# Kernel optimization log

Hardware: AMD Instinct MI355X
Metric: run time of the kernel (lower is better)

The kernel has to match this reference:

```python
import jax, jax.numpy as jnp
import numpy as np

B, S, D, H = 4, 2048, 1024, 16
HD = D // H

def setup_inputs() -> dict:
    key = jax.random.key(0)
    ks = jax.random.split(key, 11)
    s = 1.0 / np.sqrt(D)
    return {
        "q": jax.random.normal(ks[0], (B, S, D), jnp.float32),
        "k": jax.random.normal(ks[1], (B, S, D), jnp.float32),
        "v": jax.random.normal(ks[2], (B, S, D), jnp.float32),
        "Wq": jax.random.normal(ks[3], (D, D), jnp.float32) * s,
        "bq": jax.random.normal(ks[4], (D,), jnp.float32) * 0.01,
        "Wk": jax.random.normal(ks[5], (D, D), jnp.float32) * s,
        "bk": jax.random.normal(ks[6], (D,), jnp.float32) * 0.01,
        "Wv": jax.random.normal(ks[7], (D, D), jnp.float32) * s,
        "bv": jax.random.normal(ks[8], (D,), jnp.float32) * 0.01,
        "Wo": jax.random.normal(ks[9], (D, D), jnp.float32) * s,
        "bo": jax.random.normal(ks[10], (D,), jnp.float32) * 0.01,
    }

def reference(q, k, v, Wq, bq, Wk, bk, Wv, bv, Wo, bo):
    # linear projections + ReLU activation (as in the torch module)
    qh = jax.nn.relu(q @ Wq.T + bq)
    kh = jax.nn.relu(k @ Wk.T + bk)
    vh = jax.nn.relu(v @ Wv.T + bv)
    # split heads: [B,S,D] -> [B,H,S,HD]
    def split(x):
        return x.reshape(B, S, H, HD).transpose(0, 2, 1, 3)
    qh, kh, vh = split(qh), split(kh), split(vh)
    scale = 1.0 / np.sqrt(HD).astype(np.float32)
    scores = jnp.einsum("bhqd,bhkd->bhqk", qh, kh) * scale
    attn = jax.nn.softmax(scores, axis=-1)
    y = jnp.einsum("bhqk,bhkd->bhqd", attn, vh)
    # merge heads: [B,H,S,HD] -> [B,S,D]
    y = y.transpose(0, 2, 1, 3).reshape(B, S, D)
    return jax.nn.relu(y @ Wo.T + bo)
```

## Files before the change

kernel.cpp:

```cpp
#include <hip/hip_runtime.h>
#include <hip/hip_bf16.h>
#include <cstdint>
#include <cstddef>

#define Bc 4
#define Sc 2048
#define Dc 1024
#define Hc 16

typedef __bf16 bf16;
typedef bf16  bf16x4 __attribute__((ext_vector_type(4)));
typedef bf16  bf16x8 __attribute__((ext_vector_type(8)));
typedef float f32x4  __attribute__((ext_vector_type(4)));

__device__ __forceinline__ void load_lds16(const bf16* g, bf16* l) {
    __builtin_amdgcn_global_load_lds((const __attribute__((address_space(1))) void*)g,
                                     (__attribute__((address_space(3))) void*)l,
                                     16, 0, 0);
}

__device__ __forceinline__ void cvt16(const float* __restrict__ g,
                                      bf16x8& lo, bf16x8& hi) {
    const f32x4 a0 = *(const f32x4*)(g);
    const f32x4 a1 = *(const f32x4*)(g + 4);
    const f32x4 a2 = *(const f32x4*)(g + 8);
    const f32x4 a3 = *(const f32x4*)(g + 12);
#pragma unroll
    for (int j = 0; j < 4; j++) {
        lo[j]     = (bf16)a0[j];
        lo[j + 4] = (bf16)a1[j];
        hi[j]     = (bf16)a2[j];
        hi[j + 4] = (bf16)a3[j];
    }
}

__device__ __forceinline__ void store_relu(float* p, float v) { *p = fmaxf(v, 0.0f); }
__device__ __forceinline__ void store_relu(bf16*  p, float v) { *p = (bf16)fmaxf(v, 0.0f); }

__global__ __launch_bounds__(256)
void cvt_f32_bf16(const float* __restrict__ src, bf16* __restrict__ dst, int n16) {
    const int idx = blockIdx.x * 256 + threadIdx.x;
    if (idx >= n16) return;
    bf16x8 lo, hi;
    cvt16(src + (size_t)idx * 16, lo, hi);
    *(bf16x8*)(dst + (size_t)idx * 16)     = lo;
    *(bf16x8*)(dst + (size_t)idx * 16 + 8) = hi;
}

#define BM 128
#define BN 128
#define BK 64

template <typename TC, bool TR>
__global__ __launch_bounds__(256)
void gemm_bb(const bf16* __restrict__ A, const bf16* __restrict__ W,
             const float* __restrict__ bias, TC* __restrict__ C,
             int M, int N, int K) {
    constexpr int POOL = TR ? 36864 : 32768;
    __shared__ __align__(16) char pool[POOL];
    bf16* lA = (bf16*)pool;
    bf16* lB = (bf16*)(pool + 16384);

    const int t    = threadIdx.x;
    const int lane = t & 63;
    const int wave = t >> 6;
    const int l15  = lane & 15;
    const int quad = lane >> 4;

    const int m0 = blockIdx.x * BM;
    const int n0 = blockIdx.y * BN;
    const int wm = (wave >> 1) * 64;
    const int wn = (wave & 1) * 64;

    f32x4 acc[4][4] = {};

    const int srow = t >> 3;
    const int cg   = (((t & 7) ^ (srow & 7)) << 3);
    const bf16* gA = A + (size_t)(m0 + srow) * K + cg;
    const bf16* gW = W + (size_t)(n0 + srow) * K + cg;
    bf16* lA0 = lA + t * 8;
    bf16* lB0 = lB + t * 8;

    for (int k0 = 0; k0 < K; k0 += BK) {
        __syncthreads();
#pragma unroll
        for (int c = 0; c < 4; c++) {
            load_lds16(gA + (size_t)(32 * c) * K, lA0 + c * 2048);
            load_lds16(gW + (size_t)(32 * c) * K, lB0 + c * 2048);
        }
        gA += BK; gW += BK;
        __syncthreads();

#pragma unroll
        for (int ks = 0; ks < 2; ks++) {
            bf16x8 af[4], bfr[4];
#pragma unroll
            for (int mt = 0; mt < 4; mt++) {
                const int row = wm + mt * 16 + l15;
                const int colp = ((((ks << 2) | quad) ^ (l15 & 7)) << 3);
                af[mt] = *(const bf16x8*)(lA + row * BK + colp);
            }
#pragma unroll
            for (int nt = 0; nt < 4; nt++) {
                const int row = wn + nt * 16 + l15;
                const int colp = ((((ks << 2) | quad) ^ (l15 & 7)) << 3);
                bfr[nt] = *(const bf16x8*)(lB + row * BK + colp);
            }
#pragma unroll
            for (int mt = 0; mt < 4; mt++)
#pragma unroll
                for (int nt = 0; nt < 4; nt++)
                    acc[mt][nt] = __builtin_amdgcn_mfma_f32_16x16x32_bf16(
                        af[mt], bfr[nt], acc[mt][nt], 0, 0, 0);
        }
    }

    if constexpr (!TR) {
#pragma unroll
        for (int nt = 0; nt < 4; nt++) {
            const int col = n0 + wn + nt * 16 + l15;
            const float bv = bias[col];
#pragma unroll
            for (int mt = 0; mt < 4; mt++) {
                const int rowb = m0 + wm + mt * 16 + quad * 4;
#pragma unroll
                for (int i = 0; i < 4; i++)
                    store_relu(&C[(size_t)(rowb + i) * N + col], acc[mt][nt][i] + bv);
            }
        }
    } else {
        __syncthreads();
        bf16* trp = (bf16*)pool;
#pragma unroll
        for (int nt = 0; nt < 4; nt++) {
            const int col = n0 + wn + nt * 16 + l15;
            const float bv = bias[col];
#pragma unroll
            for (int mt = 0; mt < 4; mt++)
#pragma unroll
                for (int i = 0; i < 4; i++)
                    trp[((wave * 64) + nt * 16 + l15) * 72 + mt * 16 + quad * 4 + i] =
                        (bf16)fmaxf(acc[mt][nt][i] + bv, 0.0f);
        }
        __syncthreads();
        const int r2 = lane >> 3;
        const int c8 = (lane & 7) * 8;
#pragma unroll
        for (int rr = 0; rr < 8; rr++) {
            const int rt = rr * 8 + r2;
            const bf16x8 vv = *(const bf16x8*)&trp[((wave * 64) + rt) * 72 + c8];
            const int cg2 = n0 + wn + rt;
            const int h   = cg2 >> 6, hd = cg2 & 63;
            const int mg  = m0 + wm + c8;
            const int b   = mg >> 11, s = mg & (Sc - 1);
            bf16* dst = (bf16*)C + ((size_t)(b * Hc + h) * 64 + hd) * Sc + s;
            *(bf16x8*)dst = vv;
        }
    }
}

#define QI 4

__global__ __launch_bounds__(256)
void attn_flash(const bf16* __restrict__ Qh, const bf16* __restrict__ Kh,
                const bf16* __restrict__ Vt_g, bf16* __restrict__ Y) {
    __shared__ __align__(16) bf16 Kl[64][72];
    __shared__ __align__(16) bf16 Vl[64][72];
    __shared__ __align__(16) bf16 Pl[4][64][72];

    const int t    = threadIdx.x;
    const int lane = t & 63;
    const int wave = t >> 6;
    const int l15  = lane & 15;
    const int quad = lane >> 4;

    const int qt = blockIdx.x;
    const int bh = blockIdx.y;
    const int b  = bh >> 4;
    const int h  = bh & 15;
    const int q0 = qt * 256;
    const size_t rowbase = (size_t)b * Sc;
    const size_t vhead   = (size_t)(b * Hc + h) * 64;

    const float qscale = 0.125f * 1.44269504f;
    bf16x8 qf[QI][2];
#pragma unroll
    for (int qi = 0; qi < QI; qi++) {
        const bf16* qp = Qh + (rowbase + q0 + wave * 64 + qi * 16 + l15) * (size_t)Dc + h * 64;
#pragma unroll
        for (int ks = 0; ks < 2; ks++) {
            const bf16x8 raw = *(const bf16x8*)(qp + ks * 32 + quad * 8);
#pragma unroll
            for (int j = 0; j < 8; j++) qf[qi][ks][j] = (bf16)((float)raw[j] * qscale);
        }
    }

    float lrun[QI] = {};
    f32x4 yacc[QI][4] = {};

    const int sr = t >> 2;
    const int sc = (t & 3) * 16;

    for (int kt = 0; kt < Sc / 64; kt++) {
        const int kb = kt * 64;
        const bf16* kp = Kh + (rowbase + kb + sr) * (size_t)Dc + h * 64 + sc;
        const bf16* vp = Vt_g + (vhead + sr) * (size_t)Sc + kb + sc;
        const bf16x8 k0 = *(const bf16x8*)kp;
        const bf16x8 k1 = *(const bf16x8*)(kp + 8);
        const bf16x8 v0 = *(const bf16x8*)vp;
        const bf16x8 v1 = *(const bf16x8*)(vp + 8);
        __syncthreads();
        *(bf16x8*)&Kl[sr][sc]     = k0;
        *(bf16x8*)&Kl[sr][sc + 8] = k1;
        *(bf16x8*)&Vl[sr][sc]     = v0;
        *(bf16x8*)&Vl[sr][sc + 8] = v1;
        __syncthreads();

        bf16x8 kf[4][2];
#pragma unroll
        for (int mt = 0; mt < 4; mt++) {
            kf[mt][0] = *(const bf16x8*)&Kl[mt * 16 + l15][quad * 8];
            kf[mt][1] = *(const bf16x8*)&Kl[mt * 16 + l15][32 + quad * 8];
        }

#pragma unroll
        for (int qi = 0; qi < QI; qi++) {
            f32x4 s[4];
#pragma unroll
            for (int mt = 0; mt < 4; mt++) {
                s[mt] = (f32x4){0.f, 0.f, 0.f, 0.f};
                s[mt] = __builtin_amdgcn_mfma_f32_16x16x32_bf16(
                    kf[mt][0], qf[qi][0], s[mt], 0, 0, 0);
                s[mt] = __builtin_amdgcn_mfma_f32_16x16x32_bf16(
                    kf[mt][1], qf[qi][1], s[mt], 0, 0, 0);
            }
            float sum = 0.f;
#pragma unroll
            for (int mt = 0; mt < 4; mt++) {
                bf16x4 pk;
#pragma unroll
                for (int i = 0; i < 4; i++) {
                    const float p = exp2f(s[mt][i]);
                    sum += p;
                    pk[i] = (bf16)p;
                }
                *(bf16x4*)&Pl[wave][qi * 16 + l15][mt * 16 + quad * 4] = pk;
            }
            lrun[qi] += sum;
        }

        bf16x8 vf[4][2];
#pragma unroll
        for (int nt = 0; nt < 4; nt++) {
            vf[nt][0] = *(const bf16x8*)&Vl[nt * 16 + l15][quad * 8];
            vf[nt][1] = *(const bf16x8*)&Vl[nt * 16 + l15][32 + quad * 8];
        }

#pragma unroll
        for (int qi = 0; qi < QI; qi++)
#pragma unroll
            for (int ks = 0; ks < 2; ks++) {
                const bf16x8 pf = *(const bf16x8*)&Pl[wave][qi * 16 + l15][ks * 32 + quad * 8];
#pragma unroll
                for (int nt = 0; nt < 4; nt++)
                    yacc[qi][nt] = __builtin_amdgcn_mfma_f32_16x16x32_bf16(
                        vf[nt][ks], pf, yacc[qi][nt], 0, 0, 0);
            }
    }

#pragma unroll
    for (int qi = 0; qi < QI; qi++) {
        float l = lrun[qi];
        l += __shfl_xor(l, 16);
        l += __shfl_xor(l, 32);
        const float inv = 1.0f / l;
        bf16* yp = Y + (rowbase + q0 + wave * 64 + qi * 16 + l15) * (size_t)Dc + h * 64;
#pragma unroll
        for (int nt = 0; nt < 4; nt++)
#pragma unroll
            for (int i = 0; i < 4; i++)
                yp[nt * 16 + quad * 4 + i] = (bf16)(yacc[qi][nt][i] * inv);
    }
}

extern "C" void kernel_launch(void* const* d_in, const int* in_sizes, int n_in,
                              void* d_out, int out_size, void* d_ws, size_t ws_size,
                              hipStream_t stream) {
    const float* q  = (const float*)d_in[0];
    const float* k  = (const float*)d_in[1];
    const float* v  = (const float*)d_in[2];
    const float* Wq = (const float*)d_in[3];
    const float* bq = (const float*)d_in[4];
    const float* Wk = (const float*)d_in[5];
    const float* bk = (const float*)d_in[6];
    const float* Wv = (const float*)d_in[7];
    const float* bv = (const float*)d_in[8];
    const float* Wo = (const float*)d_in[9];
    const float* bo = (const float*)d_in[10];
    float* out = (float*)d_out;

    const int M = Bc * Sc;
    const int N = Dc;
    const int K = Dc;
    const size_t E  = (size_t)Bc * Sc * Dc;
    const size_t EW = (size_t)Dc * Dc;

    bf16* Qh   = (bf16*)d_out;
    bf16* Kh   = Qh + E;
    bf16* tmpA = (bf16*)d_ws;
    bf16* VtG  = tmpA + E;
    bf16* Wqb  = VtG + E;
    bf16* Wkb  = Wqb + EW;
    bf16* Wvb  = Wkb + EW;
    bf16* Wob  = Wvb + EW;

    const int n16  = (int)(E / 16);
    const int n16w = (int)(EW / 16);
    dim3 gc(n16 / 256);
    dim3 gw(n16w / 256);
    dim3 gg(M / BM, N / BN);
    dim3 ga(Sc / 256, Bc * Hc);

    cvt_f32_bf16<<<gw, 256, 0, stream>>>(Wq, Wqb, n16w);
    cvt_f32_bf16<<<gw, 256, 0, stream>>>(Wk, Wkb, n16w);
    cvt_f32_bf16<<<gw, 256, 0, stream>>>(Wv, Wvb, n16w);
    cvt_f32_bf16<<<gw, 256, 0, stream>>>(Wo, Wob, n16w);

    cvt_f32_bf16<<<gc, 256, 0, stream>>>(q, tmpA, n16);
    gemm_bb<bf16, false><<<gg, 256, 0, stream>>>(tmpA, Wqb, bq, Qh, M, N, K);

    cvt_f32_bf16<<<gc, 256, 0, stream>>>(k, tmpA, n16);
    gemm_bb<bf16, false><<<gg, 256, 0, stream>>>(tmpA, Wkb, bk, Kh, M, N, K);

    cvt_f32_bf16<<<gc, 256, 0, stream>>>(v, tmpA, n16);
    gemm_bb<bf16, true><<<gg, 256, 0, stream>>>(tmpA, Wvb, bv, VtG, M, N, K);

    attn_flash<<<ga, 256, 0, stream>>>(Qh, Kh, VtG, tmpA);

    gemm_bb<float, false><<<gg, 256, 0, stream>>>(tmpA, Wob, bo, out, M, N, K);
}
```

Measured before the change: 386.8 us.

## Interleave per-query-tile PV MFMA with softmax and compute row sums via MFMA

Restructures the flash attention inner loop so each 16-row query tile runs its QK MFMA, exp and PV MFMA back to back, using a two-slot per-wave P buffer instead of a full 64-row buffer. Row sums are now computed with an extra MFMA against a ones vector rather than scalar adds and cross-lane shuffles. The PV MFMAs are set to a higher wave priority with s_setprio. The aim is to overlap exp work with matrix work, shrink LDS use and cut VALU reductions. The cost is two extra MFMAs per tile, a row sum taken from bf16-rounded P values, and more register pressure from loading V fragments early.

```diff
diff --git a/kernel.cpp b/kernel.cpp
--- a/kernel.cpp
+++ b/kernel.cpp
@@ -166,7 +166,7 @@
                 const bf16* __restrict__ Vt_g, bf16* __restrict__ Y) {
     __shared__ __align__(16) bf16 Kl[64][72];
     __shared__ __align__(16) bf16 Vl[64][72];
-    __shared__ __align__(16) bf16 Pl[4][64][72];
+    __shared__ __align__(16) bf16 Pl[4][2][16][72];
 
     const int t    = threadIdx.x;
     const int lane = t & 63;
@@ -195,8 +195,12 @@
         }
     }
 
-    float lrun[QI] = {};
+    bf16x8 ones;
+#pragma unroll
+    for (int j = 0; j < 8; j++) ones[j] = (bf16)1.0f;
+
     f32x4 yacc[QI][4] = {};
+    f32x4 sacc[QI]    = {};
 
     const int sr = t >> 2;
     const int sc = (t & 3) * 16;
@@ -216,16 +220,23 @@
         *(bf16x8*)&Vl[sr][sc + 8] = v1;
         __syncthreads();
 
-        bf16x8 kf[4][2];
+        bf16x8 kf[4][2], vf[4][2];
 #pragma unroll
         for (int mt = 0; mt < 4; mt++) {
             kf[mt][0] = *(const bf16x8*)&Kl[mt * 16 + l15][quad * 8];
             kf[mt][1] = *(const bf16x8*)&Kl[mt * 16 + l15][32 + quad * 8];
         }
+#pragma unroll
+        for (int nt = 0; nt < 4; nt++) {
+            vf[nt][0] = *(const bf16x8*)&Vl[nt * 16 + l15][quad * 8];
+            vf[nt][1] = *(const bf16x8*)&Vl[nt * 16 + l15][32 + quad * 8];
+        }
 
 #pragma unroll
         for (int qi = 0; qi < QI; qi++) {
+            const int slot = qi & 1;
             f32x4 s[4];
+            __builtin_amdgcn_s_setprio(1);
 #pragma unroll
             for (int mt = 0; mt < 4; mt++) {
                 s[mt] = (f32x4){0.f, 0.f, 0.f, 0.f};
@@ -234,46 +245,37 @@
                 s[mt] = __builtin_amdgcn_mfma_f32_16x16x32_bf16(
                     kf[mt][1], qf[qi][1], s[mt], 0, 0, 0);
             }
-            float sum = 0.f;
+            __builtin_amdgcn_s_setprio(0);
+
 #pragma unroll
             for (int mt = 0; mt < 4; mt++) {
                 bf16x4 pk;
 #pragma unroll
-                for (int i = 0; i < 4; i++) {
-                    const float p = exp2f(s[mt][i]);
-                    sum += p;
-                    pk[i] = (bf16)p;
-                }
-                *(bf16x4*)&Pl[wave][qi * 16 + l15][mt * 16 + quad * 4] = pk;
-            }
-            lrun[qi] += sum;
-        }
-
-        bf16x8 vf[4][2];
-#pragma unroll
-        for (int nt = 0; nt < 4; nt++) {
-            vf[nt][0] = *(const bf16x8*)&Vl[nt * 16 + l15][quad * 8];
-            vf[nt][1] = *(const bf16x8*)&Vl[nt * 16 + l15][32 + quad * 8];
-        }
-
-#pragma unroll
-        for (int qi = 0; qi < QI; qi++)
-#pragma unroll
-            for (int ks = 0; ks < 2; ks++) {
-                const bf16x8 pf = *(const bf16x8*)&Pl[wave][qi * 16 + l15][ks * 32 + quad * 8];
-#pragma unroll
-                for (int nt = 0; nt < 4; nt++)
-                    yacc[qi][nt] = __builtin_amdgcn_mfma_f32_16x16x32_bf16(
-                        vf[nt][ks], pf, yacc[qi][nt], 0, 0, 0);
-            }
+                for (int i = 0; i < 4; i++)
+                    pk[i] = (bf16)exp2f(s[mt][i]);
+                *(bf16x4*)&Pl[wave][slot][l15][mt * 16 + quad * 4] = pk;
+            }
+
+            const bf16x8 pf0 = *(const bf16x8*)&Pl[wave][slot][l15][quad * 8];
+            const bf16x8 pf1 = *(const bf16x8*)&Pl[wave][slot][l15][32 + quad * 8];
+
+            __builtin_amdgcn_s_setprio(1);
+            sacc[qi] = __builtin_amdgcn_mfma_f32_16x16x32_bf16(ones, pf0, sacc[qi], 0, 0, 0);
+            sacc[qi] = __builtin_amdgcn_mfma_f32_16x16x32_bf16(ones, pf1, sacc[qi], 0, 0, 0);
+#pragma unroll
+            for (int nt = 0; nt < 4; nt++) {
+                yacc[qi][nt] = __builtin_amdgcn_mfma_f32_16x16x32_bf16(
+                    vf[nt][0], pf0, yacc[qi][nt], 0, 0, 0);
+                yacc[qi][nt] = __builtin_amdgcn_mfma_f32_16x16x32_bf16(
+                    vf[nt][1], pf1, yacc[qi][nt], 0, 0, 0);
+            }
+            __builtin_amdgcn_s_setprio(0);
+        }
     }
 
 #pragma unroll
     for (int qi = 0; qi < QI; qi++) {
-        float l = lrun[qi];
-        l += __shfl_xor(l, 16);
-        l += __shfl_xor(l, 32);
-        const float inv = 1.0f / l;
+        const float inv = 1.0f / sacc[qi][0];
         bf16* yp = Y + (rowbase + q0 + wave * 64 + qi * 16 + l15) * (size_t)Dc + h * 64;
 #pragma unroll
         for (int nt = 0; nt < 4; nt++)
```

Result: no change. 390.8 us (+1.0%).
